# Kernel optimization log

Hardware: AMD Instinct MI355X
Metric: run time of the kernel (lower is better)

The kernel has to match this reference:

```python
import jax, jax.numpy as jnp
import numpy as np

S = 20        # seq_len = obs_len(8) + pred_len(12)
G = 64        # number of groups (scenes) in the batch, from seq_start_end
NPED = 128    # pedestrians per group (equal-sized groups)
N = G * NPED
M = 200       # down-sampled boundary points per scene map (down_samples)
NSCENES = 8
MLP_DIM = 1024
COLL_THR = 0.25
OCC_THR = 1.0


def _mlp(x, w1, b1, w2, b2):
    # nn.Linear(1, mlp_dim) -> ReLU -> nn.Linear(mlp_dim, 1)
    return jnp.maximum(x @ w1 + b1, 0.0) @ w2 + b2


def _counts(traj, scenes, seq_scene_ids):
    # traj: (S, N, 2); groups are contiguous blocks of NPED pedestrians.
    x = traj.reshape(S, G, NPED, 2)
    # --- get_min_distance_agents: per-group pairwise distances ---
    # compare squared distances against thr^2 (d<thr <=> d^2<thr^2, d>=0); avoids sqrt
    diff = x[:, :, :, None, :] - x[:, :, None, :, :]            # (S,G,n,n,2)
    sq = jnp.sum(diff * diff, axis=-1)                           # (S,G,n,n)
    # distance[distance==0] = thr  =>  exact-zero distances never count
    mask_a = (sq > 0.0) & (sq < COLL_THR * COLL_THR)
    cnt_a = jnp.sum(mask_a.astype(traj.dtype), axis=(0, 2)).reshape(-1)   # (N,)
    # --- get_min_distance_scene: faithful reproduction of the original
    # scene.repeat(1, n*S).view(n*S, -1, 2) index arithmetic ---
    K = S * NPED
    pos = jnp.transpose(x, (1, 0, 2, 3)).reshape(G, K, 2)        # pos[g, t*n+ped]
    scn = scenes[seq_scene_ids]                                  # (G, M, 2)
    F = jnp.arange(K * M)
    si = F // K          # scene point index actually read by repeat/view
    pi = F // M          # flattened (t,ped) position index (X_cols_rep row)
    ped = F % NPED       # pedestrian the comparison is attributed to after .view+sum
    d2 = jnp.sum((scn[:, si, :] - pos[:, pi, :]) ** 2, axis=-1)  # (G, K*M)
    mask_s = (d2 < OCC_THR * OCC_THR).astype(traj.dtype)
    cnt_s = jax.vmap(lambda m: jax.ops.segment_sum(m, ped, num_segments=NPED))(mask_s).reshape(-1)
    return cnt_a, cnt_s


def setup_inputs() -> dict:
    key = jax.random.key(0)
    k = jax.random.split(key, 8)
    traj = jax.random.normal(k[0], (S, N, 2), dtype=jnp.float32) * 4.0
    traj_rel = jax.random.normal(k[1], (S, N, 2), dtype=jnp.float32)
    seq_start_end = jnp.stack([jnp.arange(G) * NPED, (jnp.arange(G) + 1) * NPED], axis=1).astype(jnp.int32)
    seq_scene_ids = jax.random.randint(k[2], (G,), 0, NSCENES, dtype=jnp.int32)
    scenes = jax.random.normal(k[3], (NSCENES, M, 2), dtype=jnp.float32) * 4.0
    s = 0.05
    w1a = jax.random.normal(k[4], (1, MLP_DIM), dtype=jnp.float32) * s
    b1a = jnp.zeros((MLP_DIM,), jnp.float32)
    w2a = jax.random.normal(k[5], (MLP_DIM, 1), dtype=jnp.float32) * s
    b2a = jnp.zeros((1,), jnp.float32)
    w1s = jax.random.normal(k[6], (1, MLP_DIM), dtype=jnp.float32) * s
    b1s = jnp.zeros((MLP_DIM,), jnp.float32)
    w2s = jax.random.normal(k[7], (MLP_DIM, 1), dtype=jnp.float32) * s
    b2s = jnp.zeros((1,), jnp.float32)
    return dict(traj=traj, traj_rel=traj_rel, seq_start_end=seq_start_end,
                seq_scene_ids=seq_scene_ids, scenes=scenes,
                w1a=w1a, b1a=b1a, w2a=w2a, b2a=b2a,
                w1s=w1s, b1s=b1s, w2s=w2s, b2s=b2s)


def reference(traj, traj_rel, seq_start_end, seq_scene_ids, scenes,
              w1a, b1a, w2a, b2a, w1s, b1s, w2s, b2s):
    # c_type == 'local' path of TrajectoryCritic.forward
    cnt_a, cnt_s = _counts(traj, scenes, seq_scene_ids)
    scores1 = _mlp(cnt_a[:, None], w1a, b1a, w2a, b2a)   # (N,1)
    scores2 = _mlp(cnt_s[:, None], w1s, b1s, w2s, b2s)   # (N,1)
    return (scores1, scores2)
```

## Files before the change

### kernel.cpp

```cpp
#include <hip/hip_runtime.h>

#define S_LEN 20
#define G_CNT 64
#define NPED  128
#define N_TOT 8192
#define M_PTS 200
#define MLP_DIM 1024

__global__ __launch_bounds__(512) void counts_kernel(
    const float2* __restrict__ traj,
    const int*    __restrict__ seq_scene_ids,
    const float2* __restrict__ scenes,
    int* __restrict__ partA, int* __restrict__ partS)
{
    const int bx  = blockIdx.x;
    const int g   = bx >> 2;
    const int q   = bx & 3;
    const int tid = threadIdx.x;

    __shared__ float2 P[640];
    __shared__ float2 SC[M_PTS];
    __shared__ int    red[512];
    __shared__ int    diffA[130];
    __shared__ int    baseS;

    {
        int tl = tid >> 7, ped = tid & 127;
        P[tid] = traj[(q*5 + tl)*N_TOT + g*NPED + ped];
        if (tid < 128) {
            P[512 + tid] = traj[(q*5 + 4)*N_TOT + g*NPED + tid];
        }
        int sid = seq_scene_ids[g];
        if (tid < M_PTS) SC[tid] = scenes[sid*M_PTS + tid];
        if (tid <= 128) diffA[tid] = 0;
        if (tid == 129) baseS = 0;
    }
    __syncthreads();

    {
        const unsigned thrB = __float_as_uint(0.0625f) - 1u;
        const int j = tid & 127, h = tid >> 7;
        int c = 0;
        for (int sl = 0; sl < 5; ++sl) {
            float2 xj = P[sl*128 + j];
            #pragma unroll
            for (int ii = 0; ii < 32; ++ii) {
                float2 xi = P[sl*128 + h*32 + ii];
                float dx = xj.x - xi.x;
                float dy = xj.y - xi.y;
                float sq = __fadd_rn(__fmul_rn(dx, dx), __fmul_rn(dy, dy));
                c += (int)((__float_as_uint(sq) - 1u) < thrB);
            }
        }
        red[tid] = c;
    }

    for (int pil = tid; pil < 640; pil += 512) {
        int pi = q*640 + pil;
        float2 pp = P[pil];
        int a0 = pi*200, a1 = a0 + 200;
        int s0 = a0 / 2560;
        int sL = (a1 - 1) / 2560;
        int bnd = (sL > s0) ? sL*2560 : a1;

        {
            float dx = SC[s0].x - pp.x, dy = SC[s0].y - pp.y;
            float d2 = __fadd_rn(__fmul_rn(dx, dx), __fmul_rn(dy, dy));
            if (__float_as_uint(d2) < 0x3f800000u) {
                int L = bnd - a0;
                int full = L >> 7, rem = L & 127;
                if (full) atomicAdd(&baseS, full);
                if (rem) {
                    int st = a0 & 127, en = st + rem;
                    atomicAdd(&diffA[st], 1);
                    if (en <= 128) atomicAdd(&diffA[en], -1);
                    else { atomicAdd(&diffA[0], 1); atomicAdd(&diffA[en-128], -1); }
                }
            }
        }
        if (sL > s0) {
            float dx = SC[sL].x - pp.x, dy = SC[sL].y - pp.y;
            float d2 = __fadd_rn(__fmul_rn(dx, dx), __fmul_rn(dy, dy));
            if (__float_as_uint(d2) < 0x3f800000u) {
                int L = a1 - bnd;
                int full = L >> 7, rem = L & 127;
                if (full) atomicAdd(&baseS, full);
                if (rem) {
                    int st = bnd & 127, en = st + rem;
                    atomicAdd(&diffA[st], 1);
                    if (en <= 128) atomicAdd(&diffA[en], -1);
                    else { atomicAdd(&diffA[0], 1); atomicAdd(&diffA[en-128], -1); }
                }
            }
        }
    }
    __syncthreads();

    if (tid < 128) {
        int tot = red[tid] + red[tid+128] + red[tid+256] + red[tid+384];
        partA[q*N_TOT + g*NPED + tid] = tot;

        int extra = 0;
        for (int u = 0; u < 128; ++u) {
            int dv = diffA[u];
            if (u <= tid) extra += dv;
        }
        partS[q*N_TOT + g*NPED + tid] = baseS + extra;
    }
}

__global__ __launch_bounds__(256) void mlp_kernel(
    const int* __restrict__ partA, const int* __restrict__ partS,
    const float* __restrict__ w1a, const float* __restrict__ b1a,
    const float* __restrict__ w2a, const float* __restrict__ b2a,
    const float* __restrict__ w1s, const float* __restrict__ b1s,
    const float* __restrict__ w2s, const float* __restrict__ b2s,
    float* __restrict__ out)
{
    const int bx   = blockIdx.x;
    const int tid  = threadIdx.x;
    const int lane = tid & 63;
    const int wv   = tid >> 6;
    const int o    = bx*64 + lane;
    const bool isS = (o >= N_TOT);

    const float* w1 = isS ? w1s : w1a;
    const float* b1 = isS ? b1s : b1a;
    const float* w2 = isS ? w2s : w2a;
    const float* b2 = isS ? b2s : b2a;
    const int*   pc = isS ? partS : partA;
    const int    oi = isS ? (o - N_TOT) : o;

    const int ci = pc[oi] + pc[N_TOT + oi] + pc[2*N_TOT + oi] + pc[3*N_TOT + oi];
    const float c = (float)ci;

    float acc = 0.f;
    const int k0 = wv*256;
    #pragma unroll 8
    for (int k = k0; k < k0 + 256; ++k) {
        float h = fmaxf(__fadd_rn(__fmul_rn(c, w1[k]), b1[k]), 0.f);
        acc = __fadd_rn(acc, __fmul_rn(h, w2[k]));
    }

    __shared__ float part[4][64];
    part[wv][lane] = acc;
    __syncthreads();
    if (tid < 64) {
        out[o] = part[0][tid] + part[1][tid] + part[2][tid] + part[3][tid] + b2[0];
    }
}

extern "C" void kernel_launch(void* const* d_in, const int* in_sizes, int n_in,
                              void* d_out, int out_size, void* d_ws, size_t ws_size,
                              hipStream_t stream)
{
    const float2* traj   = (const float2*)d_in[0];
    const int*    ssi    = (const int*)d_in[3];
    const float2* scenes = (const float2*)d_in[4];
    const float*  w1a    = (const float*)d_in[5];
    const float*  b1a    = (const float*)d_in[6];
    const float*  w2a    = (const float*)d_in[7];
    const float*  b2a    = (const float*)d_in[8];
    const float*  w1s    = (const float*)d_in[9];
    const float*  b1s    = (const float*)d_in[10];
    const float*  w2s    = (const float*)d_in[11];
    const float*  b2s    = (const float*)d_in[12];

    int* partA = (int*)d_ws;
    int* partS = partA + 4*N_TOT;

    counts_kernel<<<dim3(G_CNT*4), dim3(512), 0, stream>>>(traj, ssi, scenes, partA, partS);
    mlp_kernel<<<dim3(256), dim3(256), 0, stream>>>(partA, partS,
        w1a, b1a, w2a, b2a, w1s, b1s, w2s, b2s, (float*)d_out);
}
```

Baseline: 93.12 us.

## Fuse count and MLP kernels by repartitioning blocks over pedestrians

The work split changes so each block owns 32 pedestrians across all 20 timesteps instead of 5 timesteps of all 128 pedestrians. Each block therefore holds complete counts and can run both MLPs in place. The second kernel launch and the global partial-count buffers go away. In exchange, every block loads the full group trajectory and repeats the scene-comparison work for all 2560 positions, four times redundantly per group.

```diff
diff --git a/kernel.cpp b/kernel.cpp
--- a/kernel.cpp
+++ b/kernel.cpp
@@ -5,31 +5,39 @@
 #define NPED  128
 #define N_TOT 8192
 #define M_PTS 200
+#define K_GRP 2560
 #define MLP_DIM 1024
 
-__global__ __launch_bounds__(512) void counts_kernel(
+__global__ __launch_bounds__(512) void fused_kernel(
     const float2* __restrict__ traj,
     const int*    __restrict__ seq_scene_ids,
     const float2* __restrict__ scenes,
-    int* __restrict__ partA, int* __restrict__ partS)
+    const float* __restrict__ w1a, const float* __restrict__ b1a,
+    const float* __restrict__ w2a, const float* __restrict__ b2a,
+    const float* __restrict__ w1s, const float* __restrict__ b1s,
+    const float* __restrict__ w2s, const float* __restrict__ b2s,
+    float* __restrict__ out)
 {
     const int bx  = blockIdx.x;
     const int g   = bx >> 2;
     const int q   = bx & 3;
     const int tid = threadIdx.x;
 
-    __shared__ float2 P[640];
+    __shared__ float2 P[K_GRP];
     __shared__ float2 SC[M_PTS];
     __shared__ int    red[512];
     __shared__ int    diffA[130];
     __shared__ int    baseS;
+    __shared__ int    cntA[32], cntS[32];
+    __shared__ float  part[4][64];
 
+    #pragma unroll
+    for (int r = 0; r < 5; ++r) {
+        int idx = tid + r*512;
+        int t = idx >> 7, ped = idx & 127;
+        P[idx] = traj[t*N_TOT + g*NPED + ped];
+    }
     {
-        int tl = tid >> 7, ped = tid & 127;
-        P[tid] = traj[(q*5 + tl)*N_TOT + g*NPED + ped];
-        if (tid < 128) {
-            P[512 + tid] = traj[(q*5 + 4)*N_TOT + g*NPED + tid];
-        }
         int sid = seq_scene_ids[g];
         if (tid < M_PTS) SC[tid] = scenes[sid*M_PTS + tid];
         if (tid <= 128) diffA[tid] = 0;
@@ -39,13 +47,14 @@
 
     {
         const unsigned thrB = __float_as_uint(0.0625f) - 1u;
-        const int j = tid & 127, h = tid >> 7;
+        const int j = q*32 + (tid & 31);
+        const int p = tid >> 5;
         int c = 0;
-        for (int sl = 0; sl < 5; ++sl) {
+        for (int sl = 0; sl < S_LEN; ++sl) {
             float2 xj = P[sl*128 + j];
             #pragma unroll
-            for (int ii = 0; ii < 32; ++ii) {
-                float2 xi = P[sl*128 + h*32 + ii];
+            for (int ii = 0; ii < 8; ++ii) {
+                float2 xi = P[sl*128 + p*8 + ii];
                 float dx = xj.x - xi.x;
                 float dy = xj.y - xi.y;
                 float sq = __fadd_rn(__fmul_rn(dx, dx), __fmul_rn(dy, dy));
@@ -55,13 +64,12 @@
         red[tid] = c;
     }
 
-    for (int pil = tid; pil < 640; pil += 512) {
-        int pi = q*640 + pil;
+    for (int pil = tid; pil < K_GRP; pil += 512) {
         float2 pp = P[pil];
-        int a0 = pi*200, a1 = a0 + 200;
-        int s0 = a0 / 2560;
-        int sL = (a1 - 1) / 2560;
-        int bnd = (sL > s0) ? sL*2560 : a1;
+        int a0 = pil*200, a1 = a0 + 200;
+        int s0 = a0 / K_GRP;
+        int sL = (a1 - 1) / K_GRP;
+        int bnd = (sL > s0) ? sL*K_GRP : a1;
 
         {
             float dx = SC[s0].x - pp.x, dy = SC[s0].y - pp.y;
@@ -96,57 +104,49 @@
     }
     __syncthreads();
 
-    if (tid < 128) {
-        int tot = red[tid] + red[tid+128] + red[tid+256] + red[tid+384];
-        partA[q*N_TOT + g*NPED + tid] = tot;
-
-        int extra = 0;
+    if (tid < 32) {
+        int c = 0;
+        #pragma unroll
+        for (int pp = 0; pp < 16; ++pp) c += red[pp*32 + tid];
+        cntA[tid] = c;
+    }
+    if (tid >= 64 && tid < 96) {
+        int pl = tid - 64;
+        int pg = q*32 + pl;
+        int e = 0;
         for (int u = 0; u < 128; ++u) {
             int dv = diffA[u];
-            if (u <= tid) extra += dv;
+            if (u <= pg) e += dv;
         }
-        partS[q*N_TOT + g*NPED + tid] = baseS + extra;
+        cntS[pl] = baseS + e;
     }
-}
+    __syncthreads();
 
-__global__ __launch_bounds__(256) void mlp_kernel(
-    const int* __restrict__ partA, const int* __restrict__ partS,
-    const float* __restrict__ w1a, const float* __restrict__ b1a,
-    const float* __restrict__ w2a, const float* __restrict__ b2a,
-    const float* __restrict__ w1s, const float* __restrict__ b1s,
-    const float* __restrict__ w2s, const float* __restrict__ b2s,
-    float* __restrict__ out)
-{
-    const int bx   = blockIdx.x;
-    const int tid  = threadIdx.x;
-    const int lane = tid & 63;
-    const int wv   = tid >> 6;
-    const int o    = bx*64 + lane;
-    const bool isS = (o >= N_TOT);
+    if (tid < 256) {
+        const int lane = tid & 63;
+        const int wv   = tid >> 6;
+        const int m    = lane >> 5;
+        const int ped  = lane & 31;
+        const float* w1 = m ? w1s : w1a;
+        const float* b1 = m ? b1s : b1a;
+        const float* w2 = m ? w2s : w2a;
+        const float c = (float)(m ? cntS[ped] : cntA[ped]);
 
-    const float* w1 = isS ? w1s : w1a;
-    const float* b1 = isS ? b1s : b1a;
-    const float* w2 = isS ? w2s : w2a;
-    const float* b2 = isS ? b2s : b2a;
-    const int*   pc = isS ? partS : partA;
-    const int    oi = isS ? (o - N_TOT) : o;
-
-    const int ci = pc[oi] + pc[N_TOT + oi] + pc[2*N_TOT + oi] + pc[3*N_TOT + oi];
-    const float c = (float)ci;
-
-    float acc = 0.f;
-    const int k0 = wv*256;
-    #pragma unroll 8
-    for (int k = k0; k < k0 + 256; ++k) {
-        float h = fmaxf(__fadd_rn(__fmul_rn(c, w1[k]), b1[k]), 0.f);
-        acc = __fadd_rn(acc, __fmul_rn(h, w2[k]));
+        float acc = 0.f;
+        const int k0 = wv*256;
+        #pragma unroll 8
+        for (int k = k0; k < k0 + 256; ++k) {
+            float h = fmaxf(__fadd_rn(__fmul_rn(c, w1[k]), b1[k]), 0.f);
+            acc = __fadd_rn(acc, __fmul_rn(h, w2[k]));
+        }
+        part[wv][lane] = acc;
     }
-
-    __shared__ float part[4][64];
-    part[wv][lane] = acc;
     __syncthreads();
     if (tid < 64) {
-        out[o] = part[0][tid] + part[1][tid] + part[2][tid] + part[3][tid] + b2[0];
+        const int m = tid >> 5, ped = tid & 31;
+        const float b2v = m ? b2s[0] : b2a[0];
+        out[m*N_TOT + g*NPED + q*32 + ped] =
+            part[0][tid] + part[1][tid] + part[2][tid] + part[3][tid] + b2v;
     }
 }
 
@@ -166,10 +166,7 @@
     const float*  w2s    = (const float*)d_in[11];
     const float*  b2s    = (const float*)d_in[12];
 
-    int* partA = (int*)d_ws;
-    int* partS = partA + 4*N_TOT;
-
-    counts_kernel<<<dim3(G_CNT*4), dim3(512), 0, stream>>>(traj, ssi, scenes, partA, partS);
-    mlp_kernel<<<dim3(256), dim3(256), 0, stream>>>(partA, partS,
+    fused_kernel<<<dim3(G_CNT*4), dim3(512), 0, stream>>>(
+        traj, ssi, scenes,
         w1a, b1a, w2a, b2a, w1s, b1s, w2s, b2s, (float*)d_out);
 }
```

After: 91.70 us. Within noise of the previous version (-1.5%).
